# Kernel optimization log

Measured on AMD Instinct MI355X. Metric: run time of the kernel, lower is better.

The kernel has to match this reference:

```python
import jax, jax.numpy as jnp
import numpy as np

T, B, I, H = 2048, 32, 256, 256
KEEP = 0.75  # 1 - dropout_rate


def setup_inputs() -> dict:
    key = jax.random.key(0)
    ks = jax.random.split(key, 7)
    inp = jax.random.normal(ks[0], (T, B, I), dtype=jnp.float32)
    # variational dropout masks sampled once (Bernoulli(keep)), like the torch module
    zx = (jax.random.uniform(ks[1], (I,)) < KEEP).astype(jnp.float32)
    zh = (jax.random.uniform(ks[2], (H,)) < KEEP).astype(jnp.float32)
    # stacked gate weights in order [i, f, o, g]; scaled like nn.Linear default init
    s_w = 1.0 / np.sqrt(I)
    s_u = 1.0 / np.sqrt(H)
    W = jax.random.uniform(ks[3], (4 * H, I), minval=-s_w, maxval=s_w, dtype=jnp.float32)
    bW = jax.random.uniform(ks[4], (4 * H,), minval=-s_w, maxval=s_w, dtype=jnp.float32)
    U = jax.random.uniform(ks[5], (4 * H, H), minval=-s_u, maxval=s_u, dtype=jnp.float32)
    bU = jax.random.uniform(ks[6], (4 * H,), minval=-s_u, maxval=s_u, dtype=jnp.float32)
    return {"input": inp, "zx": zx, "zh": zh, "W": W, "bW": bW, "U": U, "bU": bU}


def reference(input, zx, zh, W, bW, U, bU):
    Bsz = input.shape[1]
    Hd = U.shape[1]

    def step(carry, x_t):
        h, c = carry
        x = x_t * zx          # [B, I] variational input dropout
        hm = h * zh           # [B, H] variational hidden dropout
        gates = x @ W.T + bW + hm @ U.T + bU   # [B, 4H]
        i, f, o, g = jnp.split(gates, 4, axis=-1)
        i = jax.nn.sigmoid(i)
        f = jax.nn.sigmoid(f)
        o = jax.nn.sigmoid(o)
        g = jnp.tanh(g)
        c_new = f * c + i * g
        h_new = o * jnp.tanh(c_new)
        return (h_new, c_new), h_new

    h0 = jnp.zeros((Bsz, Hd), dtype=input.dtype)
    c0 = jnp.zeros((Bsz, Hd), dtype=input.dtype)
    (h_t, c_t), hn = jax.lax.scan(step, (h0, c0), input)
    return hn, h_t, c_t
```

## Files before the change

kernel.cpp:

```cpp
#include <hip/hip_runtime.h>
#include <stdint.h>

typedef _Float16 half_t;
typedef _Float16 half2_t __attribute__((ext_vector_type(2)));

#define TSEQ 2048
#define NB   32
#define HD   256
#define HN_ELEMS ((size_t)TSEQ*NB*HD)

static __device__ __forceinline__ float fdot2u(uint32_t a, uint32_t b, float acc) {
  return __builtin_amdgcn_fdot2(__builtin_bit_cast(half2_t, a),
                                __builtin_bit_cast(half2_t, b), acc, false);
}
static __device__ __forceinline__ int sdot4(uint32_t a, uint32_t b, int c) {
#if defined(__has_builtin)
#if __has_builtin(__builtin_amdgcn_sdot4)
  return __builtin_amdgcn_sdot4((int)a, (int)b, c, false);
#else
  int d;
  asm("v_dot4_i32_i8 %0, %1, %2, %3" : "=v"(d) : "v"(a), "v"(b), "v"(c));
  return d;
#endif
#else
  int d;
  asm("v_dot4_i32_i8 %0, %1, %2, %3" : "=v"(d) : "v"(a), "v"(b), "v"(c));
  return d;
#endif
}
static __device__ __forceinline__ float sigm_f(float x) {
  return __builtin_amdgcn_rcpf(1.0f + __expf(-x));
}
static __device__ __forceinline__ float tanh_f(float x) {
  return 2.0f * __builtin_amdgcn_rcpf(1.0f + __expf(-2.0f * x)) - 1.0f;
}
static __device__ __forceinline__ signed char q8(float v, float sc) {
  int q = (int)rintf(v * sc);
  q = q > 127 ? 127 : (q < -127 ? -127 : q);
  return (signed char)q;
}

__global__ void prep_kernel(const float* __restrict__ W, const float* __restrict__ U,
                            const float* __restrict__ bW, const float* __restrict__ bU,
                            const float* __restrict__ zx, const float* __restrict__ zh,
                            half_t* __restrict__ Wpk, signed char* __restrict__ Upk3b,
                            signed char* __restrict__ Ug4b, float* __restrict__ bias,
                            half_t* __restrict__ hstate, float* __restrict__ cstate) {
  int tid = blockIdx.x * 256 + threadIdx.x;
  int n   = tid & 1023;
  int kcG = tid >> 10;
  #pragma unroll
  for (int e = 0; e < 8; ++e) {
    int k = kcG * 8 + e;
    Wpk[((size_t)kcG * 1024 + n) * 8 + e] = (half_t)(W[n * 256 + k] * zx[k]);
    float uv = U[n * 256 + k] * zh[k];
    signed char qv = q8(uv, 2032.0f);
    int kg = k >> 7, kk = k & 127, q = kk >> 4, by = kk & 15;
    if (n < 768) {
      int c = n >> 8, j = n & 255;
      Upk3b[(((size_t)(c * 2 + kg) * 8 + q) * 256 + j) * 16 + by] = qv;
    } else {
      Ug4b[(((size_t)kg * 8 + q) * 256 + (n & 255)) * 16 + by] = qv;
    }
  }
  if (kcG == 0) bias[n] = bW[n] + bU[n];
  if (tid < NB * HD) { hstate[tid] = (half_t)0.0f; cstate[tid] = 0.0f; }
}

__global__ __launch_bounds__(512)
__attribute__((amdgpu_waves_per_eu(2, 2)))
void gemm_kernel(const float* __restrict__ input, const uint4* __restrict__ Wpk,
                 const float* __restrict__ bias, half_t* __restrict__ gx, int row0) {
  __shared__ __align__(16) uint4 As[64 * 32];
  __shared__ __align__(16) uint4 pad1b[4096];
  const int tid = threadIdx.x;
  if ((int)blockIdx.x < 0) pad1b[tid] = As[tid];
  const int halfsel = blockIdx.x & 1;
  const int rbase = (blockIdx.x >> 1) * 64;
  const int col = halfsel * 512 + tid;

  uint32_t wreg[128];
  #pragma unroll
  for (int kc = 0; kc < 32; ++kc) {
    uint4 q = Wpk[(size_t)kc * 1024 + col];
    wreg[kc * 4 + 0] = q.x; wreg[kc * 4 + 1] = q.y;
    wreg[kc * 4 + 2] = q.z; wreg[kc * 4 + 3] = q.w;
  }
  const float bc = bias[col];
  #pragma unroll
  for (int i = 0; i < 8; ++i) {
    int lin = tid + i * 512;
    int row = lin >> 6, f4 = lin & 63;
    float4 v = ((const float4*)input)[((size_t)(row0 + rbase + row)) * 64 + f4];
    half2_t p0; p0[0] = (half_t)v.x; p0[1] = (half_t)v.y;
    half2_t p1; p1[0] = (half_t)v.z; p1[1] = (half_t)v.w;
    ((uint2*)As)[row * 64 + f4] = make_uint2(__builtin_bit_cast(uint32_t, p0),
                                             __builtin_bit_cast(uint32_t, p1));
  }
  __syncthreads();

  const int gate = col >> 8, j = col & 255;
  #pragma unroll 1
  for (int r = 0; r < 64; ++r) {
    const uint4* arow = As + r * 32;
    float a0 = 0.f, a1 = 0.f;
    #pragma unroll
    for (int kc = 0; kc < 16; ++kc) {
      uint4 h0 = arow[2 * kc], h1 = arow[2 * kc + 1];
      a0 = fdot2u(wreg[8 * kc + 0], h0.x, a0);
      a0 = fdot2u(wreg[8 * kc + 1], h0.y, a0);
      a0 = fdot2u(wreg[8 * kc + 2], h0.z, a0);
      a0 = fdot2u(wreg[8 * kc + 3], h0.w, a0);
      a1 = fdot2u(wreg[8 * kc + 4], h1.x, a1);
      a1 = fdot2u(wreg[8 * kc + 5], h1.y, a1);
      a1 = fdot2u(wreg[8 * kc + 6], h1.z, a1);
      a1 = fdot2u(wreg[8 * kc + 7], h1.w, a1);
    }
    gx[((size_t)(rbase + r) * HD + j) * 4 + gate] = (half_t)(a0 + a1 + bc);
  }
}

__global__ __launch_bounds__(512)
__attribute__((amdgpu_waves_per_eu(2, 2)))
void rec_kernel(const half_t* __restrict__ gx, const uint4* __restrict__ Upk3p,
                const uint4* __restrict__ Ug4p,
                half_t* __restrict__ hstate, float* __restrict__ cstate,
                float* __restrict__ out, int tbase, int TB, int last) {
  __shared__ __align__(16) uint4 uglds[4096];
  __shared__ __align__(16) signed char hbuf8[256];
  __shared__ __align__(16) int part[4 * 256];

  const int b   = blockIdx.x;
  const int tid = threadIdx.x;
  const int kg  = tid >> 8;
  const int j   = tid & 255;

  #pragma unroll
  for (int i = 0; i < 8; ++i) uglds[i * 512 + tid] = Ug4p[i * 512 + tid];

  uint32_t upk0[32], upk1[32], upk2[32];
  #pragma unroll
  for (int q = 0; q < 8; ++q) {
    uint4 v = Upk3p[((size_t)(0 * 2 + kg) * 8 + q) * 256 + j];
    upk0[q * 4 + 0] = v.x; upk0[q * 4 + 1] = v.y;
    upk0[q * 4 + 2] = v.z; upk0[q * 4 + 3] = v.w;
  }
  #pragma unroll
  for (int q = 0; q < 8; ++q) {
    uint4 v = Upk3p[((size_t)(1 * 2 + kg) * 8 + q) * 256 + j];
    upk1[q * 4 + 0] = v.x; upk1[q * 4 + 1] = v.y;
    upk1[q * 4 + 2] = v.z; upk1[q * 4 + 3] = v.w;
  }
  #pragma unroll
  for (int q = 0; q < 8; ++q) {
    uint4 v = Upk3p[((size_t)(2 * 2 + kg) * 8 + q) * 256 + j];
    upk2[q * 4 + 0] = v.x; upk2[q * 4 + 1] = v.y;
    upk2[q * 4 + 2] = v.z; upk2[q * 4 + 3] = v.w;
  }

  float cc = 0.f, hlastf = 0.f;
  uint2 gpk = make_uint2(0, 0), npk = make_uint2(0, 0);
  const uint2* gpn = (const uint2*)gx + (size_t)b * HD + j;
  float* outp = out + ((size_t)tbase * NB + b) * HD + j;
  if (kg == 0) {
    cc = cstate[b * HD + j];
    float h0 = (float)hstate[b * HD + j];
    hlastf = h0;
    hbuf8[j] = (signed char)(int)rintf(h0 * 127.0f);
    gpk = *gpn;
  }
  gpn += (size_t)NB * HD;
  __syncthreads();

  const float s = 0.0625f / 16129.0f;
  #pragma unroll 1
  for (int t = 0; t < TB; ++t) {
    if (kg == 0 && t + 1 < TB) npk = *gpn;
    gpn += (size_t)NB * HD;

    int a0 = 0, a1 = 0, a2 = 0, a3 = 0;
    const uint4* hp8 = (const uint4*)hbuf8 + kg * 8;
    const uint4* ugp = uglds + (size_t)kg * 8 * 256 + j;
    #pragma unroll
    for (int q = 0; q < 8; ++q) {
      uint4 hv = hp8[q];
      uint4 ug = ugp[q * 256];
      a0 = sdot4(upk0[q * 4 + 0], hv.x, a0);
      a0 = sdot4(upk0[q * 4 + 1], hv.y, a0);
      a0 = sdot4(upk0[q * 4 + 2], hv.z, a0);
      a0 = sdot4(upk0[q * 4 + 3], hv.w, a0);
      a1 = sdot4(upk1[q * 4 + 0], hv.x, a1);
      a1 = sdot4(upk1[q * 4 + 1], hv.y, a1);
      a1 = sdot4(upk1[q * 4 + 2], hv.z, a1);
      a1 = sdot4(upk1[q * 4 + 3], hv.w, a1);
      a2 = sdot4(upk2[q * 4 + 0], hv.x, a2);
      a2 = sdot4(upk2[q * 4 + 1], hv.y, a2);
      a2 = sdot4(upk2[q * 4 + 2], hv.z, a2);
      a2 = sdot4(upk2[q * 4 + 3], hv.w, a2);
      a3 = sdot4(ug.x, hv.x, a3);
      a3 = sdot4(ug.y, hv.y, a3);
      a3 = sdot4(ug.z, hv.z, a3);
      a3 = sdot4(ug.w, hv.w, a3);
    }
    if (kg) {
      part[0 * 256 + j] = a0;
      part[1 * 256 + j] = a1;
      part[2 * 256 + j] = a2;
      part[3 * 256 + j] = a3;
    }
    __syncthreads();
    if (kg == 0) {
      half2_t g01 = __builtin_bit_cast(half2_t, gpk.x);
      half2_t g23 = __builtin_bit_cast(half2_t, gpk.y);
      float f0 = (float)(a0 + part[0 * 256 + j]) * s + (float)g01[0];
      float f1 = (float)(a1 + part[1 * 256 + j]) * s + (float)g01[1];
      float f2 = (float)(a2 + part[2 * 256 + j]) * s + (float)g23[0];
      float f3 = (float)(a3 + part[3 * 256 + j]) * s + (float)g23[1];
      float gi = sigm_f(f0), gf = sigm_f(f1), go = sigm_f(f2), gg = tanh_f(f3);
      cc = gf * cc + gi * gg;
      float h = go * tanh_f(cc);
      hlastf = h;
      hbuf8[j] = (signed char)(int)rintf(h * 127.0f);
      *outp = h;
      if (last && t == TB - 1) {
        out[HN_ELEMS + (size_t)b * HD + j] = h;
        out[HN_ELEMS + (size_t)NB * HD + (size_t)b * HD + j] = cc;
      }
      gpk = npk;
    }
    outp += (size_t)NB * HD;
    __syncthreads();
  }
  if (kg == 0) {
    hstate[b * HD + j] = (half_t)hlastf;
    cstate[b * HD + j] = cc;
  }
}

extern "C" void kernel_launch(void* const* d_in, const int* in_sizes, int n_in,
                              void* d_out, int out_size, void* d_ws, size_t ws_size,
                              hipStream_t stream) {
  const float* input = (const float*)d_in[0];
  const float* zx    = (const float*)d_in[1];
  const float* zh    = (const float*)d_in[2];
  const float* W     = (const float*)d_in[3];
  const float* bW    = (const float*)d_in[4];
  const float* U     = (const float*)d_in[5];
  const float* bU    = (const float*)d_in[6];
  float* out = (float*)d_out;

  char* ws = (char*)d_ws;
  signed char* Upk3b = (signed char*)(ws);
  signed char* Ug4b  = (signed char*)(ws + (192 << 10));
  uint4*  Wpk    = (uint4*)(ws + (256 << 10));
  float*  bias   = (float*) (ws + (768 << 10));
  half_t* hstate = (half_t*)(ws + (772 << 10));
  float*  cstate = (float*) (ws + (788 << 10));
  half_t* gx     = (half_t*)(ws + (1 << 20));

  int TB = TSEQ;
  while (TB > 32 && (size_t)(1u << 20) + (size_t)TB * NB * 1024 * 2 > ws_size) TB >>= 1;

  prep_kernel<<<128, 256, 0, stream>>>(W, U, bW, bU, zx, zh,
                                       (half_t*)Wpk, Upk3b, Ug4b,
                                       bias, hstate, cstate);

  int nch = TSEQ / TB;
  for (int c = 0; c < nch; ++c) {
    int tbase = c * TB;
    gemm_kernel<<<(TB * NB / 64) * 2, 512, 0, stream>>>(input, Wpk, bias, gx, tbase * NB);
    rec_kernel<<<NB, 512, 0, stream>>>(gx, (const uint4*)Upk3b, (const uint4*)Ug4b,
                                       hstate, cstate, out,
                                       tbase, TB, (c == nch - 1) ? 1 : 0);
  }
}
```

Measured before the change: 2.072 ms.

## Split gemm K across half-blocks to halve weight registers and raise occupancy

The input-projection GEMM now gives each 512-thread block 256 output columns and splits K between the two halves. This halves the per-thread weight register array, and the partial sums are reduced through shared memory in groups of 8 rows. The waves_per_eu cap is removed and the block count doubles, so occupancy can rise at the cost of extra barriers and LDS traffic. A runtime XOR value (rz, derived from an input size and presumably zero) is applied to the loaded weights in both kernels, apparently to stop the compiler from rematerialising or reloading the register-resident weights.

Measured after the change: 2.034 ms. Within noise of the previous version (-1.8%).

```diff
diff --git a/kernel.cpp b/kernel.cpp
--- a/kernel.cpp
+++ b/kernel.cpp
@@ -68,23 +68,26 @@
 }
 
 __global__ __launch_bounds__(512)
-__attribute__((amdgpu_waves_per_eu(2, 2)))
 void gemm_kernel(const float* __restrict__ input, const uint4* __restrict__ Wpk,
-                 const float* __restrict__ bias, half_t* __restrict__ gx, int row0) {
-  __shared__ __align__(16) uint4 As[64 * 32];
-  __shared__ __align__(16) uint4 pad1b[4096];
+                 const float* __restrict__ bias, half_t* __restrict__ gx, int row0,
+                 uint32_t rz) {
+  __shared__ __align__(16) uint4  As[64 * 32];
+  __shared__ __align__(16) float  part[8 * 256];
+  __shared__ __align__(16) uint4  pad1b[1280];
   const int tid = threadIdx.x;
   if ((int)blockIdx.x < 0) pad1b[tid] = As[tid];
-  const int halfsel = blockIdx.x & 1;
-  const int rbase = (blockIdx.x >> 1) * 64;
-  const int col = halfsel * 512 + tid;
-
-  uint32_t wreg[128];
-  #pragma unroll
-  for (int kc = 0; kc < 32; ++kc) {
-    uint4 q = Wpk[(size_t)kc * 1024 + col];
-    wreg[kc * 4 + 0] = q.x; wreg[kc * 4 + 1] = q.y;
-    wreg[kc * 4 + 2] = q.z; wreg[kc * 4 + 3] = q.w;
+  const int cb    = blockIdx.x & 3;
+  const int rbase = (blockIdx.x >> 2) * 64;
+  const int jc    = tid & 255;
+  const int kh    = tid >> 8;
+  const int col   = cb * 256 + jc;
+
+  uint32_t wreg[64];
+  #pragma unroll
+  for (int kc = 0; kc < 16; ++kc) {
+    uint4 q = Wpk[(size_t)(kh * 16 + kc) * 1024 + col];
+    wreg[kc * 4 + 0] = q.x ^ rz; wreg[kc * 4 + 1] = q.y ^ rz;
+    wreg[kc * 4 + 2] = q.z ^ rz; wreg[kc * 4 + 3] = q.w ^ rz;
   }
   const float bc = bias[col];
   #pragma unroll
@@ -99,24 +102,36 @@
   }
   __syncthreads();
 
-  const int gate = col >> 8, j = col & 255;
   #pragma unroll 1
-  for (int r = 0; r < 64; ++r) {
-    const uint4* arow = As + r * 32;
-    float a0 = 0.f, a1 = 0.f;
+  for (int rg = 0; rg < 64; rg += 8) {
+    float acc[8];
     #pragma unroll
-    for (int kc = 0; kc < 16; ++kc) {
-      uint4 h0 = arow[2 * kc], h1 = arow[2 * kc + 1];
-      a0 = fdot2u(wreg[8 * kc + 0], h0.x, a0);
-      a0 = fdot2u(wreg[8 * kc + 1], h0.y, a0);
-      a0 = fdot2u(wreg[8 * kc + 2], h0.z, a0);
-      a0 = fdot2u(wreg[8 * kc + 3], h0.w, a0);
-      a1 = fdot2u(wreg[8 * kc + 4], h1.x, a1);
-      a1 = fdot2u(wreg[8 * kc + 5], h1.y, a1);
-      a1 = fdot2u(wreg[8 * kc + 6], h1.z, a1);
-      a1 = fdot2u(wreg[8 * kc + 7], h1.w, a1);
-    }
-    gx[((size_t)(rbase + r) * HD + j) * 4 + gate] = (half_t)(a0 + a1 + bc);
+    for (int rr = 0; rr < 8; ++rr) {
+      const uint4* arow = As + (rg + rr) * 32 + kh * 16;
+      float a = 0.f;
+      #pragma unroll
+      for (int kc = 0; kc < 16; ++kc) {
+        uint4 hv = arow[kc];
+        a = fdot2u(wreg[kc * 4 + 0], hv.x, a);
+        a = fdot2u(wreg[kc * 4 + 1], hv.y, a);
+        a = fdot2u(wreg[kc * 4 + 2], hv.z, a);
+        a = fdot2u(wreg[kc * 4 + 3], hv.w, a);
+      }
+      acc[rr] = a;
+    }
+    if (kh) {
+      #pragma unroll
+      for (int rr = 0; rr < 8; ++rr) part[rr * 256 + jc] = acc[rr];
+    }
+    __syncthreads();
+    if (!kh) {
+      #pragma unroll
+      for (int rr = 0; rr < 8; ++rr) {
+        float v = acc[rr] + part[rr * 256 + jc] + bc;
+        gx[((size_t)(rbase + rg + rr) * HD + jc) * 4 + cb] = (half_t)v;
+      }
+    }
+    __syncthreads();
   }
 }
 
@@ -125,7 +140,8 @@
 void rec_kernel(const half_t* __restrict__ gx, const uint4* __restrict__ Upk3p,
                 const uint4* __restrict__ Ug4p,
                 half_t* __restrict__ hstate, float* __restrict__ cstate,
-                float* __restrict__ out, int tbase, int TB, int last) {
+                float* __restrict__ out, int tbase, int TB, int last,
+                uint32_t rz) {
   __shared__ __align__(16) uint4 uglds[4096];
   __shared__ __align__(16) signed char hbuf8[256];
   __shared__ __align__(16) int part[4 * 256];
@@ -142,20 +158,20 @@
   #pragma unroll
   for (int q = 0; q < 8; ++q) {
     uint4 v = Upk3p[((size_t)(0 * 2 + kg) * 8 + q) * 256 + j];
-    upk0[q * 4 + 0] = v.x; upk0[q * 4 + 1] = v.y;
-    upk0[q * 4 + 2] = v.z; upk0[q * 4 + 3] = v.w;
+    upk0[q * 4 + 0] = v.x ^ rz; upk0[q * 4 + 1] = v.y ^ rz;
+    upk0[q * 4 + 2] = v.z ^ rz; upk0[q * 4 + 3] = v.w ^ rz;
   }
   #pragma unroll
   for (int q = 0; q < 8; ++q) {
     uint4 v = Upk3p[((size_t)(1 * 2 + kg) * 8 + q) * 256 + j];
-    upk1[q * 4 + 0] = v.x; upk1[q * 4 + 1] = v.y;
-    upk1[q * 4 + 2] = v.z; upk1[q * 4 + 3] = v.w;
+    upk1[q * 4 + 0] = v.x ^ rz; upk1[q * 4 + 1] = v.y ^ rz;
+    upk1[q * 4 + 2] = v.z ^ rz; upk1[q * 4 + 3] = v.w ^ rz;
   }
   #pragma unroll
   for (int q = 0; q < 8; ++q) {
     uint4 v = Upk3p[((size_t)(2 * 2 + kg) * 8 + q) * 256 + j];
-    upk2[q * 4 + 0] = v.x; upk2[q * 4 + 1] = v.y;
-    upk2[q * 4 + 2] = v.z; upk2[q * 4 + 3] = v.w;
+    upk2[q * 4 + 0] = v.x ^ rz; upk2[q * 4 + 1] = v.y ^ rz;
+    upk2[q * 4 + 2] = v.z ^ rz; upk2[q * 4 + 3] = v.w ^ rz;
   }
 
   float cc = 0.f, hlastf = 0.f;
@@ -258,6 +274,8 @@
   float*  cstate = (float*) (ws + (788 << 10));
   half_t* gx     = (half_t*)(ws + (1 << 20));
 
+  uint32_t rz = (uint32_t)(in_sizes[1] >> 9);
+
   int TB = TSEQ;
   while (TB > 32 && (size_t)(1u << 20) + (size_t)TB * NB * 1024 * 2 > ws_size) TB >>= 1;
 
@@ -268,9 +286,10 @@
   int nch = TSEQ / TB;
   for (int c = 0; c < nch; ++c) {
     int tbase = c * TB;
-    gemm_kernel<<<(TB * NB / 64) * 2, 512, 0, stream>>>(input, Wpk, bias, gx, tbase * NB);
+    gemm_kernel<<<(TB * NB / 64) * 4, 512, 0, stream>>>(input, Wpk, bias, gx,
+                                                        tbase * NB, rz);
     rec_kernel<<<NB, 512, 0, stream>>>(gx, (const uint4*)Upk3b, (const uint4*)Ug4b,
                                        hstate, cstate, out,
-                                       tbase, TB, (c == nch - 1) ? 1 : 0);
-  }
-}
+                                       tbase, TB, (c == nch - 1) ? 1 : 0, rz);
+  }
+}
```
